# Kernel optimization log

Hardware: AMD Instinct MI355X
Metric: run time of the kernel (lower is better)

Reference implementation:

```python
import jax, jax.numpy as jnp
import numpy as np
import math

B, T, C = 4, 2048, 2048
N_HEAD, N_KV = 16, 4
HD = C // N_HEAD          # 128
N_REP = N_HEAD // N_KV    # 4


def setup_inputs() -> dict:
    key = jax.random.key(0)
    ks = jax.random.split(key, 5)
    x = jax.random.normal(ks[0], (B, T, C), dtype=jnp.float32)
    s = 0.02
    wq = jax.random.normal(ks[1], (C, N_HEAD * HD), dtype=jnp.float32) * s
    wk = jax.random.normal(ks[2], (C, N_KV * HD), dtype=jnp.float32) * s
    wv = jax.random.normal(ks[3], (C, N_KV * HD), dtype=jnp.float32) * s
    wo = jax.random.normal(ks[4], (C, C), dtype=jnp.float32) * s
    # RoPE table: cos/sin pairs, equivalent to torch polar freqs_cis (theta=10000)
    inv_freq = 1.0 / (10000.0 ** (jnp.arange(0, HD, 2, dtype=jnp.float32) / HD))  # (HD/2,)
    ang = jnp.arange(T, dtype=jnp.float32)[:, None] * inv_freq[None, :]           # (T, HD/2)
    freqs_cis = jnp.stack([jnp.cos(ang), jnp.sin(ang)], axis=-1)                  # (T, HD/2, 2)
    return {"x": x, "freqs_cis": freqs_cis, "wq": wq, "wk": wk, "wv": wv, "wo": wo}


def _rope(t, freqs_cis):
    # t: (B, T, H, HD); complex multiply on (even, odd) pairs
    tp = t.reshape(*t.shape[:-1], HD // 2, 2)
    a, b = tp[..., 0], tp[..., 1]
    c = freqs_cis[: t.shape[1], :, 0][None, :, None, :]  # (1,T,1,HD/2)
    s = freqs_cis[: t.shape[1], :, 1][None, :, None, :]
    out = jnp.stack([a * c - b * s, a * s + b * c], axis=-1)
    return out.reshape(t.shape).astype(t.dtype)


def reference(x, freqs_cis, wq, wk, wv, wo):
    q = (x @ wq).reshape(B, T, N_HEAD, HD)
    k = (x @ wk).reshape(B, T, N_KV, HD)
    v = (x @ wv).reshape(B, T, N_KV, HD)
    q = _rope(q, freqs_cis)
    k = _rope(k, freqs_cis)
    # GQA attention without materializing repeated K/V: group q heads by kv head
    qg = q.reshape(B, T, N_KV, N_REP, HD)
    scale = 1.0 / math.sqrt(HD)
    att = jnp.einsum('btgrd,bsgd->bgrts', qg, k) * scale   # (B,G,R,T,S)
    causal = jnp.tril(jnp.ones((T, T), dtype=bool))
    att = jnp.where(causal, att, jnp.finfo(att.dtype).min)
    att = jax.nn.softmax(att, axis=-1)
    y = jnp.einsum('bgrts,bsgd->btgrd', att, v).reshape(B, T, C)
    y = y @ wo
    return y
```

## Files before the change

### kernel.cpp

```cpp
#include <hip/hip_runtime.h>
#include <math.h>
#include <stdint.h>

#define B_ 4
#define T_ 2048
#define C_ 2048
#define NH 16
#define NKV 4
#define HD 128
#define NREP 4
#define KVC (NKV*HD)
#define QSTR 3072

typedef __attribute__((ext_vector_type(8))) __bf16 bf16x8;
typedef __attribute__((ext_vector_type(4))) float floatx4;

#define GLOBAL_AS __attribute__((address_space(1)))
#define LDS_AS __attribute__((address_space(3)))

__device__ __forceinline__ void gl2lds16(const unsigned short* g, unsigned short* l) {
  __builtin_amdgcn_global_load_lds((const GLOBAL_AS unsigned int*)g,
                                   (LDS_AS unsigned int*)l, 16, 0, 0);
}

__device__ __forceinline__ float b2f(unsigned short u) {
  union { unsigned int i; float f; } v; v.i = ((unsigned int)u) << 16; return v.f;
}
__device__ __forceinline__ unsigned short f2b(float f) {
  union { float f; unsigned int i; } v; v.f = f;
  unsigned int r = v.i + 0x7fffu + ((v.i >> 16) & 1u);
  return (unsigned short)(r >> 16);
}

__global__ void cvt_bf16_kernel(const float* __restrict__ X,
                                unsigned short* __restrict__ Y, int n) {
  int i = (blockIdx.x * 256 + threadIdx.x) * 4;
  if (i >= n) return;
  float4 v = *(const float4*)(X + i);
  ushort4 o;
  o.x = f2b(v.x); o.y = f2b(v.y); o.z = f2b(v.z); o.w = f2b(v.w);
  *(ushort4*)(Y + i) = o;
}

__global__ void transpose_cvt_kernel(const float* __restrict__ W,
                                     unsigned short* __restrict__ Wt,
                                     int K, int N) {
  __shared__ float tile[32][33];
  int n = blockIdx.x * 32 + threadIdx.x;
  int kbase = blockIdx.y * 32;
  #pragma unroll
  for (int i = 0; i < 32; i += 8)
    tile[threadIdx.y + i][threadIdx.x] = W[(size_t)(kbase + threadIdx.y + i) * N + n];
  __syncthreads();
  int k = kbase + threadIdx.x;
  int nb = blockIdx.x * 32;
  #pragma unroll
  for (int i = 0; i < 32; i += 8)
    Wt[(size_t)(nb + threadIdx.y + i) * K + k] = f2b(tile[threadIdx.x][threadIdx.y + i]);
}

__global__ void transpose_v_kernel(const unsigned short* __restrict__ V,
                                   unsigned short* __restrict__ Vt) {
  __shared__ unsigned short tile[32][33];
  int d0 = blockIdx.x * 32;
  int sg = blockIdx.y * 32;
  int b = sg >> 11;
  int s0 = sg & (T_ - 1);
  #pragma unroll
  for (int i = 0; i < 32; i += 8)
    tile[threadIdx.y + i][threadIdx.x] =
        V[(size_t)(sg + threadIdx.y + i) * QSTR + d0 + threadIdx.x];
  __syncthreads();
  #pragma unroll
  for (int i = 0; i < 32; i += 8) {
    int d = d0 + threadIdx.y + i;
    int g = d >> 7, dl = d & 127;
    Vt[((size_t)(b * NKV + g) * HD + dl) * T_ + s0 + threadIdx.x] =
        tile[threadIdx.x][threadIdx.y + i];
  }
}

template<int STORE_BF16>
__global__ __launch_bounds__(512, 2) void gemm256_bt(
    const unsigned short* __restrict__ A,
    const unsigned short* __restrict__ Bt,
    void* __restrict__ Cout,
    int M, int N, int K)
{
  __shared__ unsigned short Lds[65536];

  int tid = threadIdx.x;

  int nbx = gridDim.x;
  int nwg = nbx * gridDim.y;
  int orig = blockIdx.y * nbx + blockIdx.x;
  int cpx = nwg >> 3;
  int swz = (orig & 7) * cpx + (orig >> 3);
  int m0 = (swz % nbx) * 256;
  int n0 = (swz / nbx) * 256;

  int wave = tid >> 6, lane = tid & 63;
  int fr = lane & 15, kg = lane >> 4;
  int slot = kg ^ ((fr >> 1) & 3);
  int wm_off = (wave >> 2) * 128;
  int wn_off = (wave & 3) * 64;

  int rowoff = wave * 16 + (lane >> 2);
  int kgs = (lane & 3) ^ ((lane >> 3) & 3);
  const unsigned short* Asrc = A  + (size_t)(m0 + rowoff) * K + kgs * 8;
  const unsigned short* Bsrc = Bt + (size_t)(n0 + rowoff) * K + kgs * 8;
  size_t rstep = (size_t)128 * K;

  int abase = (wm_off + fr) * 32 + slot * 8;
  int bbase = 8192 + (wn_off + fr) * 32 + slot * 8;

  floatx4 acc[8][4];
  #pragma unroll
  for (int i = 0; i < 8; i++)
    #pragma unroll
    for (int j = 0; j < 4; j++)
      acc[i][j] = (floatx4){0.f, 0.f, 0.f, 0.f};

  int nt = K >> 6;

  #define STAGE_HALF(tn, kkh, isB) do {                                        \
    const unsigned short* s_ = ((isB) ? Bsrc : Asrc) + (size_t)(tn) * 64 + (kkh) * 32; \
    unsigned short* d_ = &Lds[(((tn) & 1) << 15) + ((kkh) << 14) + ((isB) << 13) + (wave << 9)]; \
    gl2lds16(s_, d_);                                                          \
    gl2lds16(s_ + rstep, d_ + 4096);                                           \
  } while (0)

  STAGE_HALF(0, 0, 0); STAGE_HALF(0, 0, 1); STAGE_HALF(0, 1, 0); STAGE_HALF(0, 1, 1);
  asm volatile("s_waitcnt vmcnt(4)" ::: "memory");
  __builtin_amdgcn_s_barrier();

  bf16x8 bfrag[4];
  for (int t = 0; t < nt; ++t) {
    int cb = (t & 1) << 15;
    int more = (t + 1 < nt);
    #pragma unroll
    for (int p = 0; p < 4; ++p) {
      const int kkc = p >> 1, mhc = p & 1;
      if (mhc == 0) {
        #pragma unroll
        for (int j = 0; j < 4; ++j) {
          union { uint4 u; bf16x8 v; } tb;
          tb.u = *(const uint4*)&Lds[cb + bbase + (kkc << 14) + j * 512];
          bfrag[j] = tb.v;
        }
      }
      bf16x8 af[4];
      #pragma unroll
      for (int i = 0; i < 4; ++i) {
        union { uint4 u; bf16x8 v; } ta;
        ta.u = *(const uint4*)&Lds[cb + abase + (kkc << 14) + (mhc * 4 + i) * 512];
        af[i] = ta.v;
      }
      if (more) STAGE_HALF(t + 1, kkc, mhc);
      if (p == 1) {
        if (more) asm volatile("s_waitcnt vmcnt(4)" ::: "memory");
        else      asm volatile("s_waitcnt vmcnt(0)" ::: "memory");
      } else if (p == 3) {
        if (more) asm volatile("s_waitcnt vmcnt(4)" ::: "memory");
      }
      __builtin_amdgcn_s_barrier();
      asm volatile("s_waitcnt lgkmcnt(0)" ::: "memory");
      __builtin_amdgcn_s_setprio(1);
      #pragma unroll
      for (int i = 0; i < 4; ++i)
        #pragma unroll
        for (int j = 0; j < 4; ++j)
          acc[mhc * 4 + i][j] =
              __builtin_amdgcn_mfma_f32_16x16x32_bf16(af[i], bfrag[j], acc[mhc * 4 + i][j], 0, 0, 0);
      __builtin_amdgcn_s_setprio(0);
      __builtin_amdgcn_s_barrier();
    }
  }
  #undef STAGE_HALF

  int erow = kg * 4;
  #pragma unroll
  for (int i = 0; i < 8; ++i)
    #pragma unroll
    for (int j = 0; j < 4; ++j) {
      int gm = m0 + wm_off + i * 16 + erow;
      int gn = n0 + wn_off + j * 16 + fr;
      #pragma unroll
      for (int r = 0; r < 4; ++r) {
        float v = acc[i][j][r];
        if (STORE_BF16)
          ((unsigned short*)Cout)[(size_t)(gm + r) * N + gn] = f2b(v);
        else
          ((float*)Cout)[(size_t)(gm + r) * N + gn] = v;
      }
    }
}

__global__ void rope_kernel(unsigned short* __restrict__ X,
                            const float* __restrict__ FC, int nheads, int stride) {
  long long idx = (long long)blockIdx.x * 256 + threadIdx.x;
  int p = (int)(idx & (HD / 2 - 1));
  long long t1 = idx >> 6;
  int h = (int)(t1 % nheads);
  long long row = t1 / nheads;
  int t = (int)(row & (T_ - 1));
  float c = FC[((size_t)t * (HD / 2) + p) * 2 + 0];
  float s = FC[((size_t)t * (HD / 2) + p) * 2 + 1];
  unsigned short* ptr = X + row * (size_t)stride + h * HD + 2 * p;
  float a = b2f(ptr[0]), b = b2f(ptr[1]);
  ptr[0] = f2b(a * c - b * s);
  ptr[1] = f2b(a * s + b * c);
}

#define ABR 128
#define ABC 64
#define KLD 136
#define VLD 72
#define PLD 72

__global__ __launch_bounds__(256, 3) void attn_mfma_kernel(
    const unsigned short* __restrict__ Q,
    const unsigned short* __restrict__ Kg,
    const unsigned short* __restrict__ Vt,
    unsigned short* __restrict__ O)
{
  __shared__ unsigned short KPs[128 * PLD];
  __shared__ unsigned short Vs[HD * VLD];

  int bh = blockIdx.x;
  int qt = (int)(gridDim.y - 1 - blockIdx.y);
  int b = bh >> 4, h = bh & 15, g = h >> 2;
  int tid = threadIdx.x, wave = tid >> 6, lane = tid & 63;
  int fr = lane & 15, kg = lane >> 4, erow = 4 * kg;

  bf16x8 qf[2][4];
  #pragma unroll
  for (int rt = 0; rt < 2; rt++) {
    const unsigned short* qrow =
        Q + (size_t)(b * T_ + qt * ABR + wave * 32 + rt * 16 + fr) * QSTR + h * HD;
    #pragma unroll
    for (int kk = 0; kk < 4; kk++) {
      union { uint4 u; bf16x8 v; } t;
      t.u = *(const uint4*)(qrow + kk * 32 + kg * 8);
      qf[rt][kk] = t.v;
    }
  }

  floatx4 oacc[2][8];
  #pragma unroll
  for (int rt = 0; rt < 2; rt++)
    #pragma unroll
    for (int d = 0; d < 8; d++) oacc[rt][d] = (floatx4){0.f, 0.f, 0.f, 0.f};
  float rsum[2][4];
  #pragma unroll
  for (int rt = 0; rt < 2; rt++)
    #pragma unroll
    for (int r = 0; r < 4; r++) rsum[rt][r] = 0.f;

  const float scale = 0.08838834764831845f;
  const float MOFF = 9.0f;

  size_t krow0 = (size_t)(b * T_) * QSTR + g * HD;
  size_t vbase = ((size_t)(b * NKV + g) * HD) * T_;
  int q0 = qt * ABR + wave * 32;
  int nit = 2 * qt + 2;

  int sr = tid >> 2, kc4 = (tid & 3) * 8;
  int vr = tid >> 1, vc = (tid & 1) * 8;

  for (int it = 0; it < nit; it++) {
    int s0 = it * ABC;
    __syncthreads();
    {
      const unsigned short* src = Kg + krow0 + (size_t)(s0 + sr) * QSTR;
      #pragma unroll
      for (int c = 0; c < 4; c++)
        *(uint4*)&KPs[sr * KLD + kc4 + c * 32] = *(const uint4*)(src + kc4 + c * 32);
      const unsigned short* vsrc = Vt + vbase + (size_t)vr * T_ + s0;
      #pragma unroll
      for (int c = 0; c < 4; c++)
        *(uint4*)&Vs[vr * VLD + vc + c * 16] = *(const uint4*)(vsrc + vc + c * 16);
    }
    __syncthreads();

    floatx4 scr[2][4];
    #pragma unroll
    for (int rt = 0; rt < 2; rt++)
      #pragma unroll
      for (int t = 0; t < 4; t++) scr[rt][t] = (floatx4){0.f, 0.f, 0.f, 0.f};
    __builtin_amdgcn_s_setprio(1);
    #pragma unroll
    for (int kk = 0; kk < 4; kk++) {
      #pragma unroll
      for (int t = 0; t < 4; t++) {
        union { uint4 u; bf16x8 v; } kf;
        kf.u = *(const uint4*)&KPs[(t * 16 + fr) * KLD + kk * 32 + kg * 8];
        scr[0][t] = __builtin_amdgcn_mfma_f32_16x16x32_bf16(qf[0][kk], kf.v, scr[0][t], 0, 0, 0);
        scr[1][t] = __builtin_amdgcn_mfma_f32_16x16x32_bf16(qf[1][kk], kf.v, scr[1][t], 0, 0, 0);
      }
    }
    __builtin_amdgcn_s_setprio(0);

    #pragma unroll
    for (int t = 0; t < 4; t++) {
      int s_g = s0 + t * 16 + fr;
      #pragma unroll
      for (int rt = 0; rt < 2; rt++)
        #pragma unroll
        for (int r = 0; r < 4; r++) {
          int qrow = q0 + rt * 16 + erow + r;
          float p = (s_g <= qrow) ? __expf(scr[rt][t][r] * scale - MOFF) : 0.f;
          scr[rt][t][r] = p;
          rsum[rt][r] += p;
        }
    }
    __syncthreads();

    #pragma unroll
    for (int rt = 0; rt < 2; rt++)
      #pragma unroll
      for (int t = 0; t < 4; t++)
        #pragma unroll
        for (int r = 0; r < 4; r++)
          KPs[(wave * 32 + rt * 16 + erow + r) * PLD + t * 16 + fr] = f2b(scr[rt][t][r]);

    bf16x8 pf[2][2];
    #pragma unroll
    for (int rt = 0; rt < 2; rt++)
      #pragma unroll
      for (int kk = 0; kk < 2; kk++) {
        union { uint4 u; bf16x8 v; } t;
        t.u = *(const uint4*)&KPs[(wave * 32 + rt * 16 + fr) * PLD + kk * 32 + kg * 8];
        pf[rt][kk] = t.v;
      }
    __builtin_amdgcn_s_setprio(1);
    #pragma unroll
    for (int d = 0; d < 8; d++)
      #pragma unroll
      for (int kk = 0; kk < 2; kk++) {
        union { uint4 u; bf16x8 v; } vf;
        vf.u = *(const uint4*)&Vs[(d * 16 + fr) * VLD + kk * 32 + kg * 8];
        oacc[0][d] = __builtin_amdgcn_mfma_f32_16x16x32_bf16(pf[0][kk], vf.v, oacc[0][d], 0, 0, 0);
        oacc[1][d] = __builtin_amdgcn_mfma_f32_16x16x32_bf16(pf[1][kk], vf.v, oacc[1][d], 0, 0, 0);
      }
    __builtin_amdgcn_s_setprio(0);
  }

  #pragma unroll
  for (int rt = 0; rt < 2; rt++)
    #pragma unroll
    for (int r = 0; r < 4; r++) {
      float s = rsum[rt][r];
      s += __shfl_xor(s, 1); s += __shfl_xor(s, 2);
      s += __shfl_xor(s, 4); s += __shfl_xor(s, 8);
      rsum[rt][r] = s;
    }

  #pragma unroll
  for (int rt = 0; rt < 2; rt++)
    #pragma unroll
    for (int r = 0; r < 4; r++) {
      float inv = 1.f / rsum[rt][r];
      size_t orow =
          (size_t)(b * T_ + qt * ABR + wave * 32 + rt * 16 + erow + r) * C_ + h * HD;
      #pragma unroll
      for (int d = 0; d < 8; d++)
        O[orow + d * 16 + fr] = f2b(oacc[rt][d][r] * inv);
    }
}

extern "C" void kernel_launch(void* const* d_in, const int* in_sizes, int n_in,
                              void* d_out, int out_size, void* d_ws, size_t ws_size,
                              hipStream_t stream) {
  (void)in_sizes; (void)n_in; (void)out_size; (void)ws_size;
  const float* x  = (const float*)d_in[0];
  const float* fc = (const float*)d_in[1];
  const float* wq = (const float*)d_in[2];
  const float* wk = (const float*)d_in[3];
  const float* wv = (const float*)d_in[4];
  const float* wo = (const float*)d_in[5];
  float* out = (float*)d_out;

  char* ws = (char*)d_ws;
  unsigned short* xb   = (unsigned short*)(ws);
  unsigned short* qkv  = (unsigned short*)(ws + 33554432);
  unsigned short* wqT  = (unsigned short*)(ws + 83886080);
  unsigned short* wkT  = (unsigned short*)(ws + 92274688);
  unsigned short* wvT  = (unsigned short*)(ws + 94371840);
  unsigned short* woT  = (unsigned short*)(ws + 96468992);
  unsigned short* vt   = wqT;
  unsigned short* yb   = xb;

  int nx = B_ * T_ * C_;
  cvt_bf16_kernel<<<nx / 4 / 256, 256, 0, stream>>>(x, xb, nx);
  transpose_cvt_kernel<<<dim3(C_ / 32, C_ / 32), dim3(32, 8), 0, stream>>>(wq, wqT, C_, C_);
  transpose_cvt_kernel<<<dim3(KVC / 32, C_ / 32), dim3(32, 8), 0, stream>>>(wk, wkT, C_, KVC);
  transpose_cvt_kernel<<<dim3(KVC / 32, C_ / 32), dim3(32, 8), 0, stream>>>(wv, wvT, C_, KVC);
  transpose_cvt_kernel<<<dim3(C_ / 32, C_ / 32), dim3(32, 8), 0, stream>>>(wo, woT, C_, C_);

  int M = B_ * T_;
  gemm256_bt<1><<<dim3(M / 256, QSTR / 256), 512, 0, stream>>>(xb, wqT, qkv, M, QSTR, C_);

  long long qp = (long long)B_ * T_ * NH * (HD / 2);
  rope_kernel<<<(unsigned)(qp / 256), 256, 0, stream>>>(qkv, fc, NH, QSTR);
  long long kp = (long long)B_ * T_ * NKV * (HD / 2);
  rope_kernel<<<(unsigned)(kp / 256), 256, 0, stream>>>(qkv + 2048, fc, NKV, QSTR);

  transpose_v_kernel<<<dim3(KVC / 32, B_ * T_ / 32), dim3(32, 8), 0, stream>>>(qkv + 2560, vt);

  attn_mfma_kernel<<<dim3(B_ * NH, T_ / ABR), 256, 0, stream>>>(qkv, qkv + 2048, vt, yb);

  gemm256_bt<0><<<dim3(M / 256, C_ / 256), 512, 0, stream>>>(yb, woT, out, M, C_, C_);
}
```

Before: 532.4 us.

## Fuse prep and RoPE launches, deepen GEMM prefetch, cheapen attention softmax

Merges the x conversion and four weight transpose-conversions into one launch, and merges the Q and K RoPE kernels into one. The GEMM main loop is restructured to prefetch one and a half tiles ahead with explicit epilogue iterations, so loads overlap more with compute. Attention softmax uses exp2 with a prescaled FMA and skips the causal mask test on tiles that lie fully below the diagonal. P conversion to bf16 uses the native cast instead of manual rounding. These remove launch overhead and per-element ALU work, at the cost of more complex vmcnt bookkeeping in the GEMM pipeline.

```diff
diff --git a/kernel.cpp b/kernel.cpp
--- a/kernel.cpp
+++ b/kernel.cpp
@@ -32,31 +32,38 @@
   return (unsigned short)(r >> 16);
 }
 
-__global__ void cvt_bf16_kernel(const float* __restrict__ X,
-                                unsigned short* __restrict__ Y, int n) {
-  int i = (blockIdx.x * 256 + threadIdx.x) * 4;
-  if (i >= n) return;
-  float4 v = *(const float4*)(X + i);
-  ushort4 o;
-  o.x = f2b(v.x); o.y = f2b(v.y); o.z = f2b(v.z); o.w = f2b(v.w);
-  *(ushort4*)(Y + i) = o;
-}
-
-__global__ void transpose_cvt_kernel(const float* __restrict__ W,
-                                     unsigned short* __restrict__ Wt,
-                                     int K, int N) {
+#define NCVT 16384
+__global__ void prep_kernel(const float* __restrict__ x, unsigned short* __restrict__ xb,
+                            const float* __restrict__ wq, const float* __restrict__ wk,
+                            const float* __restrict__ wv, const float* __restrict__ wo,
+                            unsigned short* __restrict__ wqT, unsigned short* __restrict__ wkT,
+                            unsigned short* __restrict__ wvT, unsigned short* __restrict__ woT) {
   __shared__ float tile[32][33];
-  int n = blockIdx.x * 32 + threadIdx.x;
-  int kbase = blockIdx.y * 32;
+  int bid = blockIdx.x, tid = threadIdx.x;
+  if (bid < NCVT) {
+    int i = (bid * 256 + tid) * 4;
+    float4 v = *(const float4*)(x + i);
+    ushort4 o;
+    o.x = f2b(v.x); o.y = f2b(v.y); o.z = f2b(v.z); o.w = f2b(v.w);
+    *(ushort4*)(xb + i) = o;
+    return;
+  }
+  int tb = bid - NCVT;
+  const float* W; unsigned short* Wt; int N, xt, yt;
+  if (tb < 4096)      { W = wq; Wt = wqT; N = 2048; xt = tb & 63; yt = tb >> 6; }
+  else if (tb < 5120) { tb -= 4096; W = wk; Wt = wkT; N = 512; xt = tb & 15; yt = tb >> 4; }
+  else if (tb < 6144) { tb -= 5120; W = wv; Wt = wvT; N = 512; xt = tb & 15; yt = tb >> 4; }
+  else                { tb -= 6144; W = wo; Wt = woT; N = 2048; xt = tb & 63; yt = tb >> 6; }
+  int tx = tid & 31, ty = tid >> 5;
+  int n = xt * 32 + tx, kbase = yt * 32;
   #pragma unroll
   for (int i = 0; i < 32; i += 8)
-    tile[threadIdx.y + i][threadIdx.x] = W[(size_t)(kbase + threadIdx.y + i) * N + n];
+    tile[ty + i][tx] = W[(size_t)(kbase + ty + i) * N + n];
   __syncthreads();
-  int k = kbase + threadIdx.x;
-  int nb = blockIdx.x * 32;
+  int k = kbase + tx, nb = xt * 32;
   #pragma unroll
   for (int i = 0; i < 32; i += 8)
-    Wt[(size_t)(nb + threadIdx.y + i) * K + k] = f2b(tile[threadIdx.x][threadIdx.y + i]);
+    Wt[(size_t)(nb + ty + i) * C_ + k] = f2b(tile[tx][ty + i]);
 }
 
 __global__ void transpose_v_kernel(const unsigned short* __restrict__ V,
@@ -123,59 +130,75 @@
 
   int nt = K >> 6;
 
-  #define STAGE_HALF(tn, kkh, isB) do {                                        \
-    const unsigned short* s_ = ((isB) ? Bsrc : Asrc) + (size_t)(tn) * 64 + (kkh) * 32; \
-    unsigned short* d_ = &Lds[(((tn) & 1) << 15) + ((kkh) << 14) + ((isB) << 13) + (wave << 9)]; \
+  #define STAGE_HALF(tn, hh) do {                                              \
+    const unsigned short* s_ = (((hh) & 1) ? Bsrc : Asrc) + (size_t)(tn) * 64 + ((hh) >> 1) * 32; \
+    unsigned short* d_ = &Lds[(((tn) & 1) << 15) + (((hh) >> 1) << 14) + (((hh) & 1) << 13) + (wave << 9)]; \
     gl2lds16(s_, d_);                                                          \
     gl2lds16(s_ + rstep, d_ + 4096);                                           \
   } while (0)
 
-  STAGE_HALF(0, 0, 0); STAGE_HALF(0, 0, 1); STAGE_HALF(0, 1, 0); STAGE_HALF(0, 1, 1);
-  asm volatile("s_waitcnt vmcnt(4)" ::: "memory");
+  #define VMW(n) asm volatile("s_waitcnt vmcnt(" #n ")" ::: "memory")
+
+  #define PHASE(p, STG, WT) do {                                               \
+    const int kkc = (p) >> 1, mhc = (p) & 1;                                   \
+    if (mhc == 0) {                                                            \
+      _Pragma("unroll")                                                        \
+      for (int j = 0; j < 4; ++j) {                                            \
+        union { uint4 u; bf16x8 v; } tb;                                       \
+        tb.u = *(const uint4*)&Lds[cb + bbase + (kkc << 14) + j * 512];        \
+        bfrag[j] = tb.v;                                                       \
+      }                                                                        \
+    }                                                                          \
+    bf16x8 af[4];                                                              \
+    _Pragma("unroll")                                                          \
+    for (int i = 0; i < 4; ++i) {                                              \
+      union { uint4 u; bf16x8 v; } ta;                                         \
+      ta.u = *(const uint4*)&Lds[cb + abase + (kkc << 14) + (mhc * 4 + i) * 512]; \
+      af[i] = ta.v;                                                            \
+    }                                                                          \
+    STG; WT;                                                                   \
+    __builtin_amdgcn_s_barrier();                                              \
+    asm volatile("s_waitcnt lgkmcnt(0)" ::: "memory");                         \
+    __builtin_amdgcn_s_setprio(1);                                             \
+    _Pragma("unroll")                                                          \
+    for (int i = 0; i < 4; ++i)                                                \
+      _Pragma("unroll")                                                        \
+      for (int j = 0; j < 4; ++j)                                              \
+        acc[mhc * 4 + i][j] =                                                  \
+            __builtin_amdgcn_mfma_f32_16x16x32_bf16(af[i], bfrag[j], acc[mhc * 4 + i][j], 0, 0, 0); \
+    __builtin_amdgcn_s_setprio(0);                                             \
+    __builtin_amdgcn_s_barrier();                                              \
+  } while (0)
+
+  STAGE_HALF(0, 0); STAGE_HALF(0, 1); STAGE_HALF(0, 2); STAGE_HALF(0, 3);
+  STAGE_HALF(1, 0); STAGE_HALF(1, 1);
+  VMW(8);
   __builtin_amdgcn_s_barrier();
 
   bf16x8 bfrag[4];
-  for (int t = 0; t < nt; ++t) {
+  for (int t = 0; t + 2 < nt; ++t) {
     int cb = (t & 1) << 15;
-    int more = (t + 1 < nt);
-    #pragma unroll
-    for (int p = 0; p < 4; ++p) {
-      const int kkc = p >> 1, mhc = p & 1;
-      if (mhc == 0) {
-        #pragma unroll
-        for (int j = 0; j < 4; ++j) {
-          union { uint4 u; bf16x8 v; } tb;
-          tb.u = *(const uint4*)&Lds[cb + bbase + (kkc << 14) + j * 512];
-          bfrag[j] = tb.v;
-        }
-      }
-      bf16x8 af[4];
-      #pragma unroll
-      for (int i = 0; i < 4; ++i) {
-        union { uint4 u; bf16x8 v; } ta;
-        ta.u = *(const uint4*)&Lds[cb + abase + (kkc << 14) + (mhc * 4 + i) * 512];
-        af[i] = ta.v;
-      }
-      if (more) STAGE_HALF(t + 1, kkc, mhc);
-      if (p == 1) {
-        if (more) asm volatile("s_waitcnt vmcnt(4)" ::: "memory");
-        else      asm volatile("s_waitcnt vmcnt(0)" ::: "memory");
-      } else if (p == 3) {
-        if (more) asm volatile("s_waitcnt vmcnt(4)" ::: "memory");
-      }
-      __builtin_amdgcn_s_barrier();
-      asm volatile("s_waitcnt lgkmcnt(0)" ::: "memory");
-      __builtin_amdgcn_s_setprio(1);
-      #pragma unroll
-      for (int i = 0; i < 4; ++i)
-        #pragma unroll
-        for (int j = 0; j < 4; ++j)
-          acc[mhc * 4 + i][j] =
-              __builtin_amdgcn_mfma_f32_16x16x32_bf16(af[i], bfrag[j], acc[mhc * 4 + i][j], 0, 0, 0);
-      __builtin_amdgcn_s_setprio(0);
-      __builtin_amdgcn_s_barrier();
-    }
-  }
+    PHASE(0, STAGE_HALF(t + 1, 2), (void)0);
+    PHASE(1, STAGE_HALF(t + 1, 3), VMW(8));
+    PHASE(2, STAGE_HALF(t + 2, 0), (void)0);
+    PHASE(3, STAGE_HALF(t + 2, 1), VMW(8));
+  }
+  {
+    int t = nt - 2, cb = (t & 1) << 15;
+    PHASE(0, STAGE_HALF(t + 1, 2), (void)0);
+    PHASE(1, STAGE_HALF(t + 1, 3), VMW(8));
+    PHASE(2, (void)0, (void)0);
+    PHASE(3, (void)0, VMW(4));
+  }
+  {
+    int t = nt - 1, cb = (t & 1) << 15;
+    PHASE(0, (void)0, (void)0);
+    PHASE(1, (void)0, VMW(0));
+    PHASE(2, (void)0, (void)0);
+    PHASE(3, (void)0, (void)0);
+  }
+  #undef PHASE
+  #undef VMW
   #undef STAGE_HALF
 
   int erow = kg * 4;
@@ -196,17 +219,18 @@
     }
 }
 
-__global__ void rope_kernel(unsigned short* __restrict__ X,
-                            const float* __restrict__ FC, int nheads, int stride) {
+__global__ void rope_fused_kernel(unsigned short* __restrict__ X,
+                                  const float* __restrict__ FC) {
   long long idx = (long long)blockIdx.x * 256 + threadIdx.x;
   int p = (int)(idx & (HD / 2 - 1));
   long long t1 = idx >> 6;
-  int h = (int)(t1 % nheads);
-  long long row = t1 / nheads;
+  int h = (int)(t1 % (NH + NKV));
+  long long row = t1 / (NH + NKV);
   int t = (int)(row & (T_ - 1));
   float c = FC[((size_t)t * (HD / 2) + p) * 2 + 0];
   float s = FC[((size_t)t * (HD / 2) + p) * 2 + 1];
-  unsigned short* ptr = X + row * (size_t)stride + h * HD + 2 * p;
+  int off = (h < NH) ? h * HD : C_ + (h - NH) * HD;
+  unsigned short* ptr = X + row * (size_t)QSTR + off + 2 * p;
   float a = b2f(ptr[0]), b = b2f(ptr[1]);
   ptr[0] = f2b(a * c - b * s);
   ptr[1] = f2b(a * s + b * c);
@@ -257,8 +281,8 @@
     #pragma unroll
     for (int r = 0; r < 4; r++) rsum[rt][r] = 0.f;
 
-  const float scale = 0.08838834764831845f;
-  const float MOFF = 9.0f;
+  const float SC2 = 0.08838834764831845f * 1.4426950408889634f;
+  const float MO2 = 9.0f * 1.4426950408889634f;
 
   size_t krow0 = (size_t)(b * T_) * QSTR + g * HD;
   size_t vbase = ((size_t)(b * NKV + g) * HD) * T_;
@@ -301,18 +325,31 @@
     }
     __builtin_amdgcn_s_setprio(0);
 
-    #pragma unroll
-    for (int t = 0; t < 4; t++) {
-      int s_g = s0 + t * 16 + fr;
-      #pragma unroll
-      for (int rt = 0; rt < 2; rt++)
+    if (s0 + ABC - 1 <= q0) {
+      #pragma unroll
+      for (int t = 0; t < 4; t++)
         #pragma unroll
-        for (int r = 0; r < 4; r++) {
-          int qrow = q0 + rt * 16 + erow + r;
-          float p = (s_g <= qrow) ? __expf(scr[rt][t][r] * scale - MOFF) : 0.f;
-          scr[rt][t][r] = p;
-          rsum[rt][r] += p;
-        }
+        for (int rt = 0; rt < 2; rt++)
+          #pragma unroll
+          for (int r = 0; r < 4; r++) {
+            float p = exp2f(fmaf(scr[rt][t][r], SC2, -MO2));
+            scr[rt][t][r] = p;
+            rsum[rt][r] += p;
+          }
+    } else {
+      #pragma unroll
+      for (int t = 0; t < 4; t++) {
+        int s_g = s0 + t * 16 + fr;
+        #pragma unroll
+        for (int rt = 0; rt < 2; rt++)
+          #pragma unroll
+          for (int r = 0; r < 4; r++) {
+            int qrow = q0 + rt * 16 + erow + r;
+            float p = (s_g <= qrow) ? exp2f(fmaf(scr[rt][t][r], SC2, -MO2)) : 0.f;
+            scr[rt][t][r] = p;
+            rsum[rt][r] += p;
+          }
+      }
     }
     __syncthreads();
 
@@ -322,7 +359,8 @@
       for (int t = 0; t < 4; t++)
         #pragma unroll
         for (int r = 0; r < 4; r++)
-          KPs[(wave * 32 + rt * 16 + erow + r) * PLD + t * 16 + fr] = f2b(scr[rt][t][r]);
+          ((__bf16*)KPs)[(wave * 32 + rt * 16 + erow + r) * PLD + t * 16 + fr] =
+              (__bf16)scr[rt][t][r];
 
     bf16x8 pf[2][2];
     #pragma unroll
@@ -391,20 +429,14 @@
   unsigned short* vt   = wqT;
   unsigned short* yb   = xb;
 
-  int nx = B_ * T_ * C_;
-  cvt_bf16_kernel<<<nx / 4 / 256, 256, 0, stream>>>(x, xb, nx);
-  transpose_cvt_kernel<<<dim3(C_ / 32, C_ / 32), dim3(32, 8), 0, stream>>>(wq, wqT, C_, C_);
-  transpose_cvt_kernel<<<dim3(KVC / 32, C_ / 32), dim3(32, 8), 0, stream>>>(wk, wkT, C_, KVC);
-  transpose_cvt_kernel<<<dim3(KVC / 32, C_ / 32), dim3(32, 8), 0, stream>>>(wv, wvT, C_, KVC);
-  transpose_cvt_kernel<<<dim3(C_ / 32, C_ / 32), dim3(32, 8), 0, stream>>>(wo, woT, C_, C_);
+  prep_kernel<<<NCVT + 10240, 256, 0, stream>>>(x, xb, wq, wk, wv, wo,
+                                                wqT, wkT, wvT, woT);
 
   int M = B_ * T_;
   gemm256_bt<1><<<dim3(M / 256, QSTR / 256), 512, 0, stream>>>(xb, wqT, qkv, M, QSTR, C_);
 
-  long long qp = (long long)B_ * T_ * NH * (HD / 2);
-  rope_kernel<<<(unsigned)(qp / 256), 256, 0, stream>>>(qkv, fc, NH, QSTR);
-  long long kp = (long long)B_ * T_ * NKV * (HD / 2);
-  rope_kernel<<<(unsigned)(kp / 256), 256, 0, stream>>>(qkv + 2048, fc, NKV, QSTR);
+  long long rp = (long long)B_ * T_ * (NH + NKV) * (HD / 2);
+  rope_fused_kernel<<<(unsigned)(rp / 256), 256, 0, stream>>>(qkv, fc);
 
   transpose_v_kernel<<<dim3(KVC / 32, B_ * T_ / 32), dim3(32, 8), 0, stream>>>(qkv + 2560, vt);
 
```

Measured after the change: 569.3 us. 6.9% more time.
